# Performance work log

Measured on AMD Instinct MI355X. Metric: run time of the kernel, lower is better.

## Reference

```python
import jax, jax.numpy as jnp
import numpy as np

B, S_NEW, D = 2, 1024, 2048
CACHE_LEN = 4096
H, KVH, HD = 32, 8, 64
REP = H // KVH  # 4
POS = 3072


def setup_inputs() -> dict:
    key = jax.random.key(0)
    ks = jax.random.split(key, 11)
    sc = 0.02
    return {
        "x": jax.random.normal(ks[0], (B, S_NEW, D), jnp.float32),
        "k_cache": jax.random.normal(ks[1], (B, CACHE_LEN, KVH, HD), jnp.float32),
        "v_cache": jax.random.normal(ks[2], (B, CACHE_LEN, KVH, HD), jnp.float32),
        "Wq": jax.random.normal(ks[3], (D, H * HD), jnp.float32) * sc,
        "bq": jax.random.normal(ks[4], (H * HD,), jnp.float32) * sc,
        "Wk": jax.random.normal(ks[5], (D, KVH * HD), jnp.float32) * sc,
        "bk": jax.random.normal(ks[6], (KVH * HD,), jnp.float32) * sc,
        "Wv": jax.random.normal(ks[7], (D, KVH * HD), jnp.float32) * sc,
        "bv": jax.random.normal(ks[8], (KVH * HD,), jnp.float32) * sc,
        "Wo": jax.random.normal(ks[9], (H * HD, D), jnp.float32) * sc,
        "bo": jax.random.normal(ks[10], (D,), jnp.float32) * sc,
        "input_pos": POS,
    }


def reference(x, k_cache, v_cache, Wq, bq, Wk, bk, Wv, bv, Wo, bo, input_pos):
    b, s, _ = x.shape
    # projections
    q = (x @ Wq + bq).reshape(b, s, H, HD)
    k = (x @ Wk + bk).reshape(b, s, KVH, HD)
    v = (x @ Wv + bv).reshape(b, s, KVH, HD)
    # KV-cache append (input_pos is a static Python int)
    k_cache = jax.lax.dynamic_update_slice(k_cache, k, (0, input_pos, 0, 0))
    v_cache = jax.lax.dynamic_update_slice(v_cache, v, (0, input_pos, 0, 0))
    T = input_pos + s
    ck = k_cache[:b, :T]  # [b, T, KVH, HD]
    cv = v_cache[:b, :T]
    # GQA: query head h attends with kv head h // REP -> group q as [b, KVH, REP, s, HD]
    qg = q.reshape(b, s, KVH, REP, HD)
    scale = 1.0 / np.sqrt(HD).astype(np.float32)
    # scores: [b, KVH, REP, s, T]
    scores = jnp.einsum("bsgrd,btgd->bgrst", qg, ck) * scale
    weights = jax.nn.softmax(scores, axis=-1)
    # out: [b, KVH, REP, s, HD] -> [b, s, H*HD]
    z = jnp.einsum("bgrst,btgd->bsgrd", weights, cv).reshape(b, s, H * HD)
    return z @ Wo + bo
```

## Files before the change

kernel.cpp:

```cpp
#include <hip/hip_runtime.h>

#define BB   2
#define SS   1024
#define DD   2048
#define CL   4096
#define HH   32
#define KVH  8
#define HD   64
#define POS  3072
#define TTOT 4096
#define NQKV 3072

typedef __bf16 bfv8 __attribute__((ext_vector_type(8)));
typedef __bf16 bfv4 __attribute__((ext_vector_type(4)));
typedef unsigned short usv8 __attribute__((ext_vector_type(8)));
typedef unsigned short usv4 __attribute__((ext_vector_type(4)));
typedef float f32x4 __attribute__((ext_vector_type(4)));

#define QSCALE 0.18033688011112042f

static __device__ __forceinline__ unsigned short f2bf(float f) {
  return __builtin_bit_cast(unsigned short, (__bf16)f);
}

static __device__ __forceinline__ float fexp2(float x) {
  float r;
  asm("v_exp_f32 %0, %1" : "=v"(r) : "v"(x));
  return r;
}

static __device__ __forceinline__ f32x4 mfma16(bfv8 a, bfv8 b, f32x4 c) {
  return __builtin_amdgcn_mfma_f32_16x16x32_bf16(a, b, c, 0, 0, 0);
}

static __device__ __forceinline__ void gload16(const unsigned short* g, unsigned short* l) {
  typedef const __attribute__((address_space(1))) unsigned int GU;
  typedef __attribute__((address_space(3))) unsigned int LU;
  __builtin_amdgcn_global_load_lds((GU*)(unsigned long long)(uintptr_t)g,
                                   (LU*)(unsigned int)(uintptr_t)l, 16, 0, 0);
}

#define WAIT_VM0_BARRIER() do { \
  asm volatile("s_waitcnt vmcnt(0)" : : : "memory"); \
  __builtin_amdgcn_s_barrier(); } while (0)

__global__ __launch_bounds__(256) void conv_x_kernel(
    const float* __restrict__ x, const float* __restrict__ bq,
    const float* __restrict__ bk, const float* __restrict__ bv,
    unsigned short* __restrict__ xb, float* __restrict__ biasws) {
  int gid = blockIdx.x * 256 + threadIdx.x;
  if (gid < NQKV)
    biasws[gid] = gid < 2048 ? bq[gid] : (gid < 2560 ? bk[gid - 2048] : bv[gid - 2560]);
  f32x4 v = reinterpret_cast<const f32x4*>(x)[gid];
  usv4 o;
#pragma unroll
  for (int e = 0; e < 4; ++e) o[e] = f2bf(v[e]);
  reinterpret_cast<usv4*>(xb)[gid] = o;
}

__global__ __launch_bounds__(256) void trw_kernel(const float* __restrict__ src, int Ns,
                                                  unsigned short* __restrict__ dst) {
  __shared__ unsigned short L[64][72];
  const int n0 = blockIdx.x * 64, k0 = blockIdx.y * 64;
  const int tid = threadIdx.x;
#pragma unroll
  for (int p = 0; p < 4; ++p) {
    int r = p * 16 + (tid >> 4), c4 = tid & 15;
    f32x4 v = *reinterpret_cast<const f32x4*>(src + (long)(k0 + r) * Ns + n0 + c4 * 4);
#pragma unroll
    for (int e = 0; e < 4; ++e) L[r][c4 * 4 + e] = f2bf(v[e]);
  }
  __syncthreads();
  int n = tid >> 2, kc = (tid & 3) * 16;
  usv8 a, b;
#pragma unroll
  for (int e = 0; e < 8; ++e) { a[e] = L[kc + e][n]; b[e] = L[kc + 8 + e][n]; }
  unsigned short* dp = dst + (long)(n0 + n) * DD + k0 + kc;
  *reinterpret_cast<usv8*>(dp) = a;
  *reinterpret_cast<usv8*>(dp + 8) = b;
}

__global__ __launch_bounds__(256) void kcopy_kernel(const float* __restrict__ kc,
                                                    unsigned short* __restrict__ Kb) {
  int i = blockIdx.x * 256 + threadIdx.x;
  const int PERB = POS * KVH * 16;
  int b = i / PERB, rem = i - b * PERB;
  int t = rem / (KVH * 16), r2 = rem - t * (KVH * 16);
  int g = r2 >> 4, d4 = r2 & 15;
  f32x4 v = reinterpret_cast<const f32x4*>(kc)[(((long)((b * CL + t) * KVH + g)) << 4) + d4];
  usv4 o;
#pragma unroll
  for (int e = 0; e < 4; ++e) o[e] = f2bf(v[e]);
  reinterpret_cast<usv4*>(Kb)[(((long)((b * KVH + g) * CL + t)) << 4) + d4] = o;
}

__global__ __launch_bounds__(256) void vtrans_kernel(const float* __restrict__ vc,
                                                     unsigned short* __restrict__ Vb) {
  __shared__ unsigned short L[64][72];
  const int t0 = (blockIdx.x % 48) * 64;
  const int g = (blockIdx.x / 48) % KVH;
  const int b = blockIdx.x / (48 * KVH);
  const int tid = threadIdx.x;
  const int r = tid >> 2;
#pragma unroll
  for (int p = 0; p < 4; ++p) {
    int f = (tid & 3) + p * 4;
    f32x4 v = reinterpret_cast<const f32x4*>(vc)[(((long)(b * CL + t0 + r) * KVH + g) << 4) + f];
#pragma unroll
    for (int e = 0; e < 4; ++e) L[r][f * 4 + e] = f2bf(v[e]);
  }
  __syncthreads();
  int d = tid >> 2, tc = (tid & 3) * 16;
  usv8 a, b8;
#pragma unroll
  for (int e = 0; e < 8; ++e) { a[e] = L[tc + e][d]; b8[e] = L[tc + 8 + e][d]; }
  unsigned short* dp = Vb + (((long)((b * KVH + g) * HD + d)) << 12) + t0 + tc;
  *reinterpret_cast<usv8*>(dp) = a;
  *reinterpret_cast<usv8*>(dp + 8) = b8;
}

template <int MODE>
__global__ __launch_bounds__(256) void gemm2_kernel(
    const unsigned short* __restrict__ A, const unsigned short* __restrict__ Bt,
    const float* __restrict__ bias, float* __restrict__ outp,
    unsigned short* __restrict__ qout, unsigned short* __restrict__ kout,
    unsigned short* __restrict__ vout, int N, int K) {
  __shared__ unsigned short Al[2][64 * 32];
  __shared__ unsigned short Bl[2][128 * 32];
  const int tid = threadIdx.x;
  const int lane = tid & 63, w = tid >> 6;
  const int lr = lane & 15, lg = lane >> 4;
  const int wr = (w & 1) * 32, wc = (w >> 1) * 64;
  const int m0 = blockIdx.y * 64, n0 = blockIdx.x * 128;
  f32x4 acc[2][4];
#pragma unroll
  for (int a = 0; a < 2; ++a)
#pragma unroll
    for (int c = 0; c < 4; ++c) acc[a][c] = (f32x4){0.f, 0.f, 0.f, 0.f};

  const unsigned short* ga = A + (long)(m0 + 16 * w + (lane >> 2)) * K + (lane & 3) * 8;
  const unsigned short* gb = Bt + (long)(n0 + 32 * w + (lane >> 2)) * K + (lane & 3) * 8;
  unsigned short* const Al0 = &Al[0][0];
  unsigned short* const Al1 = &Al[1][0];
  unsigned short* const Bl0 = &Bl[0][0];
  unsigned short* const Bl1 = &Bl[1][0];
  const int wa = w * 512, wb = w * 1024;

  gload16(ga,          Al0 + wa);
  gload16(gb,          Bl0 + wb);
  gload16(gb + 16 * K, Bl0 + wb + 512);

  const int NIT = K >> 5;
  for (int it = 0; it < NIT; ++it) {
    WAIT_VM0_BARRIER();
    const bool odd = it & 1;
    const unsigned short* Ard = odd ? Al1 : Al0;
    const unsigned short* Brd = odd ? Bl1 : Bl0;
    if (it + 1 < NIT) {
      int kn = (it + 1) * 32;
      unsigned short* ad = (odd ? Al0 : Al1) + wa;
      unsigned short* bd = (odd ? Bl0 : Bl1) + wb;
      gload16(ga + kn,          ad);
      gload16(gb + kn,          bd);
      gload16(gb + kn + 16 * K, bd + 512);
    }
    bfv8 af[2], bf_[4];
#pragma unroll
    for (int mi = 0; mi < 2; ++mi)
      af[mi] = *reinterpret_cast<const bfv8*>(Ard + (wr + mi * 16 + lr) * 32 + lg * 8);
#pragma unroll
    for (int ni = 0; ni < 4; ++ni)
      bf_[ni] = *reinterpret_cast<const bfv8*>(Brd + (wc + ni * 16 + lr) * 32 + lg * 8);
#pragma unroll
    for (int mi = 0; mi < 2; ++mi)
#pragma unroll
      for (int ni = 0; ni < 4; ++ni)
        acc[mi][ni] = mfma16(af[mi], bf_[ni], acc[mi][ni]);
    __builtin_amdgcn_s_barrier();
  }

#pragma unroll
  for (int mi = 0; mi < 2; ++mi) {
#pragma unroll
    for (int ni = 0; ni < 4; ++ni) {
      int gn = n0 + wc + ni * 16 + lr;
      float bvl = bias[gn];
      float vals[4];
#pragma unroll
      for (int j = 0; j < 4; ++j) vals[j] = acc[mi][ni][j] + bvl;
      int gmb = m0 + wr + mi * 16 + lg * 4;
      if constexpr (MODE == 1) {
#pragma unroll
        for (int j = 0; j < 4; ++j) outp[(long)(gmb + j) * N + gn] = vals[j];
      } else {
        int b = gmb >> 10, s = gmb & 1023;
        if (gn < 2048) {
          int h = gn >> 6, d = gn & 63;
#pragma unroll
          for (int j = 0; j < 4; ++j)
            qout[(((long)((b * HH + h) * SS + s + j)) << 6) + d] = f2bf(vals[j] * QSCALE);
        } else if (gn < 2560) {
          int g = (gn - 2048) >> 6, d = gn & 63;
#pragma unroll
          for (int j = 0; j < 4; ++j)
            kout[(((long)((b * KVH + g) * CL + POS + s + j)) << 6) + d] = f2bf(vals[j]);
        } else {
          int g = (gn - 2560) >> 6, d = gn & 63;
          usv4 o;
#pragma unroll
          for (int j = 0; j < 4; ++j) o[j] = f2bf(vals[j]);
          *reinterpret_cast<usv4*>(vout + (((long)((b * KVH + g) * HD + d)) << 12) + POS + s) = o;
        }
      }
    }
  }
}

__global__ __launch_bounds__(256) void attn_kernel(
    const unsigned short* __restrict__ Q, const unsigned short* __restrict__ Kb,
    const unsigned short* __restrict__ Vb, unsigned short* __restrict__ Z) {
  __shared__ unsigned short Kl[2 * 64 * 64];
  __shared__ unsigned short Vl[2 * 64 * 64];
  __shared__ unsigned short Pl[4 * 16 * 64];

  const int tid = threadIdx.x;
  const int lane = tid & 63, w = tid >> 6;
  const int lr = lane & 15, lg = lane >> 4;
  const int s0 = blockIdx.x * 64;
  const int h = blockIdx.y, b = blockIdx.z, g = h >> 2;
  const int sw = s0 + w * 16;
  const int woff = w * 1024;

  const unsigned short* qb = Q + (((long)((b * HH + h) * SS + sw + lr)) << 6) + lg * 8;
  bfv8 qf0 = *reinterpret_cast<const bfv8*>(qb);
  bfv8 qf1 = *reinterpret_cast<const bfv8*>(qb + 32);

  const unsigned short* kg = Kb + (((long)(b * KVH + g)) << 18);
  const unsigned short* vg = Vb + (((long)(b * KVH + g)) << 18);

  const int rw = lane >> 3;
  const int ug = (lane & 7) ^ rw;
  const unsigned short* kA = kg + (16 * w + rw) * 64 + ug * 8;
  const unsigned short* vA = vg + (long)(16 * w + rw) * TTOT + ug * 8;

  unsigned short* const Kl0 = Kl;
  unsigned short* const Kl1 = Kl + 4096;
  unsigned short* const Vl0 = Vl;
  unsigned short* const Vl1 = Vl + 4096;

  const int sz = lr & 7;
  const int u0 = (lg ^ sz) * 8, u1 = ((lg ^ sz) ^ 4) * 8;

  const int swzP = (lr & 7) << 3;
  unsigned short* const prow = Pl + (w * 16 + lr) * 64;
  const int p0 = (lg * 8) ^ swzP, p1 = (32 + lg * 8) ^ swzP;

  f32x4 O[4];
#pragma unroll
  for (int dt = 0; dt < 4; ++dt) O[dt] = (f32x4){0.f, 0.f, 0.f, 0.f};
  float lsum = 0.f;

  gload16(kA,            Kl0 + woff);
  gload16(kA + 8 * 64,   Kl0 + woff + 512);
  gload16(vA,            Vl0 + woff);
  gload16(vA + 8 * TTOT, Vl0 + woff + 512);

  for (int it = 0; it < 64; ++it) {
    WAIT_VM0_BARRIER();
    const bool odd = it & 1;
    const unsigned short* krd = odd ? Kl1 : Kl0;
    const unsigned short* vrd = odd ? Vl1 : Vl0;
    if (it < 63) {
      int tn = (it + 1) * 64;
      unsigned short* kwd = (odd ? Kl0 : Kl1) + woff;
      unsigned short* vwd = (odd ? Vl0 : Vl1) + woff;
      gload16(kA + tn * 64,           kwd);
      gload16(kA + tn * 64 + 8 * 64,  kwd + 512);
      gload16(vA + tn,                vwd);
      gload16(vA + tn + 8 * TTOT,     vwd + 512);
    }

    __builtin_amdgcn_s_setprio(1);
    f32x4 sv[4];
#pragma unroll
    for (int tt = 0; tt < 4; ++tt) {
      const unsigned short* kr = krd + (tt * 16 + lr) * 64;
      bfv8 kf0 = *reinterpret_cast<const bfv8*>(kr + u0);
      bfv8 kf1 = *reinterpret_cast<const bfv8*>(kr + u1);
      f32x4 z = (f32x4){0.f, 0.f, 0.f, 0.f};
      z = mfma16(kf0, qf0, z);
      z = mfma16(kf1, qf1, z);
      sv[tt] = z;
    }
    __builtin_amdgcn_s_setprio(0);

    float ps = 0.f;
#pragma unroll
    for (int tt = 0; tt < 4; ++tt)
#pragma unroll
      for (int j = 0; j < 4; ++j) {
        float p = fexp2(sv[tt][j]);
        sv[tt][j] = p;
        ps += p;
      }
    lsum += ps;

#pragma unroll
    for (int tt = 0; tt < 4; ++tt) {
      bfv4 pv;
#pragma unroll
      for (int j = 0; j < 4; ++j) pv[j] = (__bf16)sv[tt][j];
      *reinterpret_cast<bfv4*>(&prow[(tt * 16 + lg * 4) ^ swzP]) = pv;
    }

    bfv8 pf0 = *reinterpret_cast<const bfv8*>(&prow[p0]);
    bfv8 pf1 = *reinterpret_cast<const bfv8*>(&prow[p1]);
    __builtin_amdgcn_s_setprio(1);
#pragma unroll
    for (int dt = 0; dt < 4; ++dt) {
      const unsigned short* vr = vrd + (dt * 16 + lr) * 64;
      bfv8 vf0 = *reinterpret_cast<const bfv8*>(vr + u0);
      bfv8 vf1 = *reinterpret_cast<const bfv8*>(vr + u1);
      O[dt] = mfma16(pf0, vf0, O[dt]);
      O[dt] = mfma16(pf1, vf1, O[dt]);
    }
    __builtin_amdgcn_s_setprio(0);
    __builtin_amdgcn_s_barrier();
  }

  lsum += __shfl_xor(lsum, 16);
  lsum += __shfl_xor(lsum, 32);
  float lj[4];
#pragma unroll
  for (int j = 0; j < 4; ++j) lj[j] = 1.0f / __shfl(lsum, lg * 4 + j);
#pragma unroll
  for (int dt = 0; dt < 4; ++dt)
#pragma unroll
    for (int j = 0; j < 4; ++j) {
      int s = sw + lg * 4 + j, d = dt * 16 + lr;
      Z[(((long)(b * SS + s)) << 11) + h * 64 + d] = f2bf(O[dt][j] * lj[j]);
    }
}

extern "C" void kernel_launch(void* const* d_in, const int* in_sizes, int n_in,
                              void* d_out, int out_size, void* d_ws, size_t ws_size,
                              hipStream_t stream) {
  const float* x  = (const float*)d_in[0];
  const float* kc = (const float*)d_in[1];
  const float* vc = (const float*)d_in[2];
  const float* Wq = (const float*)d_in[3];
  const float* bq = (const float*)d_in[4];
  const float* Wk = (const float*)d_in[5];
  const float* bk = (const float*)d_in[6];
  const float* Wv = (const float*)d_in[7];
  const float* bv = (const float*)d_in[8];
  const float* Wo = (const float*)d_in[9];
  const float* bo = (const float*)d_in[10];

  unsigned short* Kb    = (unsigned short*)d_ws;
  unsigned short* Vb    = Kb + 4194304;
  unsigned short* q_ws  = Vb + 4194304;
  unsigned short* xb    = q_ws + 4194304;
  unsigned short* z_ws  = xb;
  unsigned short* Wqkvt = xb + 4194304;
  unsigned short* Wot   = Wqkvt + 6291456;
  float* biasws = (float*)(Wot + 4194304);

  conv_x_kernel<<<4096, 256, 0, stream>>>(x, bq, bk, bv, xb, biasws);
  trw_kernel<<<dim3(32, 32), 256, 0, stream>>>(Wq, 2048, Wqkvt);
  trw_kernel<<<dim3(8, 32), 256, 0, stream>>>(Wk, 512, Wqkvt + (long)2048 * 2048);
  trw_kernel<<<dim3(8, 32), 256, 0, stream>>>(Wv, 512, Wqkvt + (long)2560 * 2048);
  trw_kernel<<<dim3(32, 32), 256, 0, stream>>>(Wo, 2048, Wot);
  kcopy_kernel<<<3072, 256, 0, stream>>>(kc, Kb);
  vtrans_kernel<<<768, 256, 0, stream>>>(vc, Vb);
  gemm2_kernel<0><<<dim3(24, 32), 256, 0, stream>>>(xb, Wqkvt, biasws, nullptr,
                                                    q_ws, Kb, Vb, NQKV, DD);
  attn_kernel<<<dim3(16, 32, 2), 256, 0, stream>>>(q_ws, Kb, Vb, z_ws);
  gemm2_kernel<1><<<dim3(16, 32), 256, 0, stream>>>(z_ws, Wot, bo, (float*)d_out,
                                                    nullptr, nullptr, nullptr, DD, DD);
}
```

Before: 321.2 us.

## Fuse prep kernels, triple-buffer GEMM loads, widen attention blocks to share K/V tiles

Merges the seven conversion and transpose kernels into one launch that dispatches on block index, which removes per-launch overhead and tail gaps. The projection GEMM moves from double to triple-buffered LDS staging with a partial vmcnt wait. It also drops the trailing barrier and raises MFMA priority so loads two steps ahead overlap compute. Attention blocks grow to 512 threads covering 128 queries, so each K/V tile loaded into LDS serves twice as many waves, and its trailing barrier is dropped too. The cost is more LDS per block and larger blocks, which may lower occupancy.

```diff
diff --git a/kernel.cpp b/kernel.cpp
--- a/kernel.cpp
+++ b/kernel.cpp
@@ -44,79 +44,85 @@
   asm volatile("s_waitcnt vmcnt(0)" : : : "memory"); \
   __builtin_amdgcn_s_barrier(); } while (0)
 
-__global__ __launch_bounds__(256) void conv_x_kernel(
+__global__ __launch_bounds__(256) void prep_kernel(
     const float* __restrict__ x, const float* __restrict__ bq,
     const float* __restrict__ bk, const float* __restrict__ bv,
-    unsigned short* __restrict__ xb, float* __restrict__ biasws) {
-  int gid = blockIdx.x * 256 + threadIdx.x;
-  if (gid < NQKV)
-    biasws[gid] = gid < 2048 ? bq[gid] : (gid < 2560 ? bk[gid - 2048] : bv[gid - 2560]);
-  f32x4 v = reinterpret_cast<const f32x4*>(x)[gid];
-  usv4 o;
-#pragma unroll
-  for (int e = 0; e < 4; ++e) o[e] = f2bf(v[e]);
-  reinterpret_cast<usv4*>(xb)[gid] = o;
-}
-
-__global__ __launch_bounds__(256) void trw_kernel(const float* __restrict__ src, int Ns,
-                                                  unsigned short* __restrict__ dst) {
+    const float* __restrict__ kc, const float* __restrict__ vc,
+    const float* __restrict__ Wq, const float* __restrict__ Wk,
+    const float* __restrict__ Wv, const float* __restrict__ Wo,
+    unsigned short* __restrict__ xb, float* __restrict__ biasws,
+    unsigned short* __restrict__ Kb, unsigned short* __restrict__ Vb,
+    unsigned short* __restrict__ Wqkvt, unsigned short* __restrict__ Wot) {
   __shared__ unsigned short L[64][72];
-  const int n0 = blockIdx.x * 64, k0 = blockIdx.y * 64;
   const int tid = threadIdx.x;
-#pragma unroll
-  for (int p = 0; p < 4; ++p) {
-    int r = p * 16 + (tid >> 4), c4 = tid & 15;
-    f32x4 v = *reinterpret_cast<const f32x4*>(src + (long)(k0 + r) * Ns + n0 + c4 * 4);
-#pragma unroll
-    for (int e = 0; e < 4; ++e) L[r][c4 * 4 + e] = f2bf(v[e]);
+  const int bid = blockIdx.x;
+  if (bid < 4096) {
+    int gid = bid * 256 + tid;
+    if (gid < NQKV)
+      biasws[gid] = gid < 2048 ? bq[gid] : (gid < 2560 ? bk[gid - 2048] : bv[gid - 2560]);
+    f32x4 v = reinterpret_cast<const f32x4*>(x)[gid];
+    usv4 o;
+#pragma unroll
+    for (int e = 0; e < 4; ++e) o[e] = f2bf(v[e]);
+    reinterpret_cast<usv4*>(xb)[gid] = o;
+  } else if (bid < 6656) {
+    int idx = bid - 4096;
+    int bx = idx % 80, k0 = (idx / 80) * 64;
+    const float* src;
+    unsigned short* dst;
+    int Ns, n0;
+    if (bx < 32)      { src = Wq; Ns = 2048; dst = Wqkvt;                     n0 = bx * 64; }
+    else if (bx < 40) { src = Wk; Ns = 512;  dst = Wqkvt + (long)2048 * 2048; n0 = (bx - 32) * 64; }
+    else if (bx < 48) { src = Wv; Ns = 512;  dst = Wqkvt + (long)2560 * 2048; n0 = (bx - 40) * 64; }
+    else              { src = Wo; Ns = 2048; dst = Wot;                       n0 = (bx - 48) * 64; }
+#pragma unroll
+    for (int p = 0; p < 4; ++p) {
+      int r = p * 16 + (tid >> 4), c4 = tid & 15;
+      f32x4 v = *reinterpret_cast<const f32x4*>(src + (long)(k0 + r) * Ns + n0 + c4 * 4);
+#pragma unroll
+      for (int e = 0; e < 4; ++e) L[r][c4 * 4 + e] = f2bf(v[e]);
+    }
+    __syncthreads();
+    int n = tid >> 2, kc_ = (tid & 3) * 16;
+    usv8 a, b;
+#pragma unroll
+    for (int e = 0; e < 8; ++e) { a[e] = L[kc_ + e][n]; b[e] = L[kc_ + 8 + e][n]; }
+    unsigned short* dp = dst + (long)(n0 + n) * DD + k0 + kc_;
+    *reinterpret_cast<usv8*>(dp) = a;
+    *reinterpret_cast<usv8*>(dp + 8) = b;
+  } else if (bid < 9728) {
+    int i = (bid - 6656) * 256 + tid;
+    const int PERB = POS * KVH * 16;
+    int b = i / PERB, rem = i - b * PERB;
+    int t = rem / (KVH * 16), r2 = rem - t * (KVH * 16);
+    int g = r2 >> 4, d4 = r2 & 15;
+    f32x4 v = reinterpret_cast<const f32x4*>(kc)[(((long)((b * CL + t) * KVH + g)) << 4) + d4];
+    usv4 o;
+#pragma unroll
+    for (int e = 0; e < 4; ++e) o[e] = f2bf(v[e]);
+    reinterpret_cast<usv4*>(Kb)[(((long)((b * KVH + g) * CL + t)) << 4) + d4] = o;
+  } else {
+    const int vb = bid - 9728;
+    const int t0 = (vb % 48) * 64;
+    const int g = (vb / 48) % KVH;
+    const int b = vb / (48 * KVH);
+    const int r = tid >> 2;
+#pragma unroll
+    for (int p = 0; p < 4; ++p) {
+      int f = (tid & 3) + p * 4;
+      f32x4 v = reinterpret_cast<const f32x4*>(vc)[(((long)(b * CL + t0 + r) * KVH + g) << 4) + f];
+#pragma unroll
+      for (int e = 0; e < 4; ++e) L[r][f * 4 + e] = f2bf(v[e]);
+    }
+    __syncthreads();
+    int d = tid >> 2, tc = (tid & 3) * 16;
+    usv8 a, b8;
+#pragma unroll
+    for (int e = 0; e < 8; ++e) { a[e] = L[tc + e][d]; b8[e] = L[tc + 8 + e][d]; }
+    unsigned short* dp = Vb + (((long)((b * KVH + g) * HD + d)) << 12) + t0 + tc;
+    *reinterpret_cast<usv8*>(dp) = a;
+    *reinterpret_cast<usv8*>(dp + 8) = b8;
   }
-  __syncthreads();
-  int n = tid >> 2, kc = (tid & 3) * 16;
-  usv8 a, b;
-#pragma unroll
-  for (int e = 0; e < 8; ++e) { a[e] = L[kc + e][n]; b[e] = L[kc + 8 + e][n]; }
-  unsigned short* dp = dst + (long)(n0 + n) * DD + k0 + kc;
-  *reinterpret_cast<usv8*>(dp) = a;
-  *reinterpret_cast<usv8*>(dp + 8) = b;
-}
-
-__global__ __launch_bounds__(256) void kcopy_kernel(const float* __restrict__ kc,
-                                                    unsigned short* __restrict__ Kb) {
-  int i = blockIdx.x * 256 + threadIdx.x;
-  const int PERB = POS * KVH * 16;
-  int b = i / PERB, rem = i - b * PERB;
-  int t = rem / (KVH * 16), r2 = rem - t * (KVH * 16);
-  int g = r2 >> 4, d4 = r2 & 15;
-  f32x4 v = reinterpret_cast<const f32x4*>(kc)[(((long)((b * CL + t) * KVH + g)) << 4) + d4];
-  usv4 o;
-#pragma unroll
-  for (int e = 0; e < 4; ++e) o[e] = f2bf(v[e]);
-  reinterpret_cast<usv4*>(Kb)[(((long)((b * KVH + g) * CL + t)) << 4) + d4] = o;
-}
-
-__global__ __launch_bounds__(256) void vtrans_kernel(const float* __restrict__ vc,
-                                                     unsigned short* __restrict__ Vb) {
-  __shared__ unsigned short L[64][72];
-  const int t0 = (blockIdx.x % 48) * 64;
-  const int g = (blockIdx.x / 48) % KVH;
-  const int b = blockIdx.x / (48 * KVH);
-  const int tid = threadIdx.x;
-  const int r = tid >> 2;
-#pragma unroll
-  for (int p = 0; p < 4; ++p) {
-    int f = (tid & 3) + p * 4;
-    f32x4 v = reinterpret_cast<const f32x4*>(vc)[(((long)(b * CL + t0 + r) * KVH + g) << 4) + f];
-#pragma unroll
-    for (int e = 0; e < 4; ++e) L[r][f * 4 + e] = f2bf(v[e]);
-  }
-  __syncthreads();
-  int d = tid >> 2, tc = (tid & 3) * 16;
-  usv8 a, b8;
-#pragma unroll
-  for (int e = 0; e < 8; ++e) { a[e] = L[tc + e][d]; b8[e] = L[tc + 8 + e][d]; }
-  unsigned short* dp = Vb + (((long)((b * KVH + g) * HD + d)) << 12) + t0 + tc;
-  *reinterpret_cast<usv8*>(dp) = a;
-  *reinterpret_cast<usv8*>(dp + 8) = b8;
 }
 
 template <int MODE>
@@ -125,8 +131,8 @@
     const float* __restrict__ bias, float* __restrict__ outp,
     unsigned short* __restrict__ qout, unsigned short* __restrict__ kout,
     unsigned short* __restrict__ vout, int N, int K) {
-  __shared__ unsigned short Al[2][64 * 32];
-  __shared__ unsigned short Bl[2][128 * 32];
+  __shared__ unsigned short Al[3][64 * 32];
+  __shared__ unsigned short Bl[3][128 * 32];
   const int tid = threadIdx.x;
   const int lane = tid & 63, w = tid >> 6;
   const int lr = lane & 15, lg = lane >> 4;
@@ -140,30 +146,24 @@
 
   const unsigned short* ga = A + (long)(m0 + 16 * w + (lane >> 2)) * K + (lane & 3) * 8;
   const unsigned short* gb = Bt + (long)(n0 + 32 * w + (lane >> 2)) * K + (lane & 3) * 8;
-  unsigned short* const Al0 = &Al[0][0];
-  unsigned short* const Al1 = &Al[1][0];
-  unsigned short* const Bl0 = &Bl[0][0];
-  unsigned short* const Bl1 = &Bl[1][0];
   const int wa = w * 512, wb = w * 1024;
 
-  gload16(ga,          Al0 + wa);
-  gload16(gb,          Bl0 + wb);
-  gload16(gb + 16 * K, Bl0 + wb + 512);
+#define STAGE_G(k) do { int kn_ = (k) * 32, b3_ = (k) % 3;          \
+    gload16(ga + kn_,          &Al[b3_][wa]);                       \
+    gload16(gb + kn_,          &Bl[b3_][wb]);                       \
+    gload16(gb + kn_ + 16 * K, &Bl[b3_][wb + 512]); } while (0)
+
+  STAGE_G(0);
+  STAGE_G(1);
 
   const int NIT = K >> 5;
   for (int it = 0; it < NIT; ++it) {
-    WAIT_VM0_BARRIER();
-    const bool odd = it & 1;
-    const unsigned short* Ard = odd ? Al1 : Al0;
-    const unsigned short* Brd = odd ? Bl1 : Bl0;
-    if (it + 1 < NIT) {
-      int kn = (it + 1) * 32;
-      unsigned short* ad = (odd ? Al0 : Al1) + wa;
-      unsigned short* bd = (odd ? Bl0 : Bl1) + wb;
-      gload16(ga + kn,          ad);
-      gload16(gb + kn,          bd);
-      gload16(gb + kn + 16 * K, bd + 512);
-    }
+    if (it + 1 < NIT) asm volatile("s_waitcnt vmcnt(3)" : : : "memory");
+    else              asm volatile("s_waitcnt vmcnt(0)" : : : "memory");
+    __builtin_amdgcn_s_barrier();
+    if (it + 2 < NIT) STAGE_G(it + 2);
+    const unsigned short* Ard = &Al[it % 3][0];
+    const unsigned short* Brd = &Bl[it % 3][0];
     bfv8 af[2], bf_[4];
 #pragma unroll
     for (int mi = 0; mi < 2; ++mi)
@@ -171,13 +171,15 @@
 #pragma unroll
     for (int ni = 0; ni < 4; ++ni)
       bf_[ni] = *reinterpret_cast<const bfv8*>(Brd + (wc + ni * 16 + lr) * 32 + lg * 8);
+    __builtin_amdgcn_s_setprio(1);
 #pragma unroll
     for (int mi = 0; mi < 2; ++mi)
 #pragma unroll
       for (int ni = 0; ni < 4; ++ni)
         acc[mi][ni] = mfma16(af[mi], bf_[ni], acc[mi][ni]);
-    __builtin_amdgcn_s_barrier();
+    __builtin_amdgcn_s_setprio(0);
   }
+#undef STAGE_G
 
 #pragma unroll
   for (int mi = 0; mi < 2; ++mi) {
@@ -216,20 +218,19 @@
   }
 }
 
-__global__ __launch_bounds__(256) void attn_kernel(
+__global__ __launch_bounds__(512) void attn_kernel(
     const unsigned short* __restrict__ Q, const unsigned short* __restrict__ Kb,
     const unsigned short* __restrict__ Vb, unsigned short* __restrict__ Z) {
   __shared__ unsigned short Kl[2 * 64 * 64];
   __shared__ unsigned short Vl[2 * 64 * 64];
-  __shared__ unsigned short Pl[4 * 16 * 64];
+  __shared__ unsigned short Pl[8 * 16 * 64];
 
   const int tid = threadIdx.x;
   const int lane = tid & 63, w = tid >> 6;
   const int lr = lane & 15, lg = lane >> 4;
-  const int s0 = blockIdx.x * 64;
   const int h = blockIdx.y, b = blockIdx.z, g = h >> 2;
-  const int sw = s0 + w * 16;
-  const int woff = w * 1024;
+  const int sw = blockIdx.x * 128 + (w >> 2) * 64 + (w & 3) * 16;
+  const int woff = w * 512;
 
   const unsigned short* qb = Q + (((long)((b * HH + h) * SS + sw + lr)) << 6) + lg * 8;
   bfv8 qf0 = *reinterpret_cast<const bfv8*>(qb);
@@ -240,8 +241,8 @@
 
   const int rw = lane >> 3;
   const int ug = (lane & 7) ^ rw;
-  const unsigned short* kA = kg + (16 * w + rw) * 64 + ug * 8;
-  const unsigned short* vA = vg + (long)(16 * w + rw) * TTOT + ug * 8;
+  const unsigned short* kA = kg + (8 * w + rw) * 64 + ug * 8;
+  const unsigned short* vA = vg + (long)(8 * w + rw) * TTOT + ug * 8;
 
   unsigned short* const Kl0 = Kl;
   unsigned short* const Kl1 = Kl + 4096;
@@ -260,10 +261,8 @@
   for (int dt = 0; dt < 4; ++dt) O[dt] = (f32x4){0.f, 0.f, 0.f, 0.f};
   float lsum = 0.f;
 
-  gload16(kA,            Kl0 + woff);
-  gload16(kA + 8 * 64,   Kl0 + woff + 512);
-  gload16(vA,            Vl0 + woff);
-  gload16(vA + 8 * TTOT, Vl0 + woff + 512);
+  gload16(kA, Kl0 + woff);
+  gload16(vA, Vl0 + woff);
 
   for (int it = 0; it < 64; ++it) {
     WAIT_VM0_BARRIER();
@@ -272,12 +271,8 @@
     const unsigned short* vrd = odd ? Vl1 : Vl0;
     if (it < 63) {
       int tn = (it + 1) * 64;
-      unsigned short* kwd = (odd ? Kl0 : Kl1) + woff;
-      unsigned short* vwd = (odd ? Vl0 : Vl1) + woff;
-      gload16(kA + tn * 64,           kwd);
-      gload16(kA + tn * 64 + 8 * 64,  kwd + 512);
-      gload16(vA + tn,                vwd);
-      gload16(vA + tn + 8 * TTOT,     vwd + 512);
+      gload16(kA + tn * 64, (odd ? Kl0 : Kl1) + woff);
+      gload16(vA + tn,      (odd ? Vl0 : Vl1) + woff);
     }
 
     __builtin_amdgcn_s_setprio(1);
@@ -325,7 +320,6 @@
       O[dt] = mfma16(pf1, vf1, O[dt]);
     }
     __builtin_amdgcn_s_setprio(0);
-    __builtin_amdgcn_s_barrier();
   }
 
   lsum += __shfl_xor(lsum, 16);
@@ -366,16 +360,11 @@
   unsigned short* Wot   = Wqkvt + 6291456;
   float* biasws = (float*)(Wot + 4194304);
 
-  conv_x_kernel<<<4096, 256, 0, stream>>>(x, bq, bk, bv, xb, biasws);
-  trw_kernel<<<dim3(32, 32), 256, 0, stream>>>(Wq, 2048, Wqkvt);
-  trw_kernel<<<dim3(8, 32), 256, 0, stream>>>(Wk, 512, Wqkvt + (long)2048 * 2048);
-  trw_kernel<<<dim3(8, 32), 256, 0, stream>>>(Wv, 512, Wqkvt + (long)2560 * 2048);
-  trw_kernel<<<dim3(32, 32), 256, 0, stream>>>(Wo, 2048, Wot);
-  kcopy_kernel<<<3072, 256, 0, stream>>>(kc, Kb);
-  vtrans_kernel<<<768, 256, 0, stream>>>(vc, Vb);
+  prep_kernel<<<10496, 256, 0, stream>>>(x, bq, bk, bv, kc, vc, Wq, Wk, Wv, Wo,
+                                         xb, biasws, Kb, Vb, Wqkvt, Wot);
   gemm2_kernel<0><<<dim3(24, 32), 256, 0, stream>>>(xb, Wqkvt, biasws, nullptr,
                                                     q_ws, Kb, Vb, NQKV, DD);
-  attn_kernel<<<dim3(16, 32, 2), 256, 0, stream>>>(q_ws, Kb, Vb, z_ws);
+  attn_kernel<<<dim3(8, 32, 2), 512, 0, stream>>>(q_ws, Kb, Vb, z_ws);
   gemm2_kernel<1><<<dim3(16, 32), 256, 0, stream>>>(z_ws, Wot, bo, (float*)d_out,
                                                     nullptr, nullptr, nullptr, DD, DD);
 }
```

Result: faster. 295.9 us (-7.9%).
